# Kernel optimization log

Measured on AMD Instinct MI355X. Metric: run time of the kernel, lower is better.

The kernel has to match this reference:

```python
import math
import jax, jax.numpy as jnp
import numpy as np

I_DIM = 64
N_MODES = 16
FACTOR = 4
EPS = 1e-5


def group_norm(x, w, b):
    # x: [B, M, N, C] channels-last; torch GroupNorm(C//16, C) over (group_channels, M, N)
    B, M, N, C = x.shape
    g = C // 16
    xr = x.reshape(B, M, N, g, C // g)
    mean = xr.mean(axis=(1, 2, 4), keepdims=True)
    var = xr.var(axis=(1, 2, 4), keepdims=True)
    xr = (xr - mean) * jax.lax.rsqrt(var + EPS)
    return xr.reshape(B, M, N, C) * w + b


def feed_forward(x, res, l1w, l1b, l2w, l2b, g1w, g1b, g2w, g2b, g3w, g3b):
    h = x @ l1w + l1b                      # [B,M,N,C*factor]
    h = group_norm(h, g1w, g1b)            # fork_1
    h = jax.nn.relu(h)
    h = h @ l2w + l2b                      # [B,M,N,C]
    h = group_norm(h, g2w, g2b)            # fork_2
    h = res + h
    h = group_norm(h, g3w, g3b)            # fork_3
    return h


def setup_inputs() -> dict:
    key = jax.random.key(0)
    ks = jax.random.split(key, 20)
    B, M, N, I = 4, 128, 128, I_DIM
    H = I * FACTOR
    z = jax.random.normal(ks[0], (B, 2 * M * N * I, 1), dtype=jnp.float32)
    x = jax.random.normal(ks[1], (B, M * N * I, 1), dtype=jnp.float32)
    # fourier weights [in, out, nm, nm, 2], xavier-ish scale
    fw_scale = math.sqrt(2.0 / (I + I))
    fw1 = jax.random.normal(ks[2], (I, I, N_MODES, N_MODES, 2), dtype=jnp.float32) * fw_scale
    fw2 = jax.random.normal(ks[3], (I, I, N_MODES, N_MODES, 2), dtype=jnp.float32) * fw_scale
    def ff_params(k0):
        kk = jax.random.split(k0, 4)
        return dict(
            l1w=jax.random.normal(kk[0], (I, H), dtype=jnp.float32) * math.sqrt(2.0 / (I + H)),
            l1b=jnp.zeros((H,), jnp.float32),
            l2w=jax.random.normal(kk[1], (H, I), dtype=jnp.float32) * math.sqrt(2.0 / (I + H)),
            l2b=jnp.zeros((I,), jnp.float32),
            g1w=jnp.ones((H,), jnp.float32), g1b=jnp.zeros((H,), jnp.float32),
            g2w=jnp.ones((I,), jnp.float32), g2b=jnp.zeros((I,), jnp.float32),
            g3w=jnp.ones((I,), jnp.float32), g3b=jnp.zeros((I,), jnp.float32),
        )
    bp = ff_params(ks[4])
    fp = ff_params(ks[5])
    out = {"z": z, "x": x, "fw1": fw1, "fw2": fw2}
    for name, p in (("b", bp), ("f", fp)):
        for k, v in p.items():
            out[f"{name}_{k}"] = v
    return out


def reference(z, x, fw1, fw2,
              b_l1w, b_l1b, b_l2w, b_l2b, b_g1w, b_g1b, b_g2w, b_g2b, b_g3w, b_g3b,
              f_l1w, f_l1b, f_l2w, f_l2b, f_g1w, f_g1b, f_g2w, f_g2b, f_g3w, f_g3b):
    I = I_DIM
    nm = N_MODES
    B = x.shape[0]
    M = N = int(math.sqrt(x.shape[1] // I))
    x4 = x.reshape(B, M, N, I)
    z5 = z.reshape(B, 2, M, N, I)
    backcast, forecast = z5[:, 0], z5[:, 1]
    x4 = x4 - backcast
    xc = jnp.transpose(x4, (0, 3, 1, 2))          # [B, I, M, N]
    x_ft = jnp.fft.rfft2(xc, s=(M, N), norm='ortho')  # [B, I, M, N//2+1] complex64
    w1 = fw1[..., 0] + 1j * fw1[..., 1]
    w2 = fw2[..., 0] + 1j * fw2[..., 1]
    top = jnp.einsum('bixy,ioxy->boxy', x_ft[:, :, :nm, :nm], w1)
    bot = jnp.einsum('bixy,ioxy->boxy', x_ft[:, :, -nm:, :nm], w2)
    out_ft = jnp.zeros((B, I, N, M // 2 + 1), dtype=x_ft.dtype)
    out_ft = out_ft.at[:, :, :nm, :nm].set(top).at[:, :, -nm:, :nm].set(bot)
    xo = jnp.fft.irfft2(out_ft, s=(N, M), norm='ortho')  # [B, I, M, N]
    xo = jnp.transpose(xo, (0, 2, 3, 1))                  # [B, M, N, I]
    backcast = feed_forward(xo, backcast, b_l1w, b_l1b, b_l2w, b_l2b,
                            b_g1w, b_g1b, b_g2w, b_g2b, b_g3w, b_g3b)
    forecast = feed_forward(xo, forecast, f_l1w, f_l1b, f_l2w, f_l2b,
                            f_g1w, f_g1b, f_g2w, f_g2b, f_g3w, f_g3b)
    out = jnp.stack([backcast, forecast], axis=1)         # [B, 2, M, N, I]
    return out.reshape(B, 2 * M * N * I, 1)
```

## Files before the change

kernel.cpp:

```cpp
#include <hip/hip_runtime.h>
#include <hip/hip_bf16.h>

typedef __hip_bfloat16 bf16;
typedef __attribute__((ext_vector_type(8))) short short8;
typedef __attribute__((ext_vector_type(4))) float f32x4;

#define PI2 6.283185307179586f
#define EPSV 1e-5f

__device__ __forceinline__ short f2bs(float f){
  bf16 h = __float2bfloat16(f);
  short s; __builtin_memcpy(&s, &h, 2); return s;
}
__device__ __forceinline__ float s2f(short s){
  bf16 h; __builtin_memcpy(&h, &s, 2); return __bfloat162float(h);
}

__global__ __launch_bounds__(256) void k_prep(
    const float* __restrict__ fw1, const float* __restrict__ fw2,
    float2* __restrict__ FWT,
    const float* __restrict__ b_l1w, const float* __restrict__ b_l1b,
    const float* __restrict__ b_l2w, const float* __restrict__ b_l2b,
    const float* __restrict__ b_g1w, const float* __restrict__ b_g1b,
    const float* __restrict__ b_g2w, const float* __restrict__ b_g2b,
    const float* __restrict__ b_g3w, const float* __restrict__ b_g3b,
    const float* __restrict__ f_l1w, const float* __restrict__ f_l1b,
    const float* __restrict__ f_l2w, const float* __restrict__ f_l2b,
    const float* __restrict__ f_g1w, const float* __restrict__ f_g1b,
    const float* __restrict__ f_g2w, const float* __restrict__ f_g2b,
    const float* __restrict__ f_g3w, const float* __restrict__ f_g3b,
    short* __restrict__ W1g, short* __restrict__ W2g,
    float2* __restrict__ TWY, float2* __restrict__ TWX,
    float* __restrict__ PB, float* __restrict__ ST){
  __shared__ float Ls[16][512];
  int tid = threadIdx.x;
  if(blockIdx.x < 512){
    int arr = blockIdx.x >> 8, rem = blockIdx.x & 255;
    int i = rem >> 2, o0 = (rem & 3) * 16;
    const float* src = (arr ? fw2 : fw1) + ((size_t)(i*64 + o0))*512;
    for(int idx = tid; idx < 8192; idx += 256)
      Ls[idx >> 9][idx & 511] = src[idx];
    __syncthreads();
    int kxw = tid >> 4, ky = tid & 15;
    float2* dst = FWT + ((size_t)((arr*16 + kxw)*16 + ky))*4096 + i*64 + o0;
    for(int ol = 0; ol < 16; ol++)
      dst[ol] = make_float2(Ls[ol][tid*2], Ls[ol][tid*2 + 1]);
    return;
  }
  int i = (blockIdx.x - 512)*256 + tid;
  if(i < 32768){
    int br = i >> 14, r = i & 16383;
    int fid = r >> 9, lane = (r >> 3) & 63, e = r & 7;
    int hb = fid & 1, t = (fid >> 1) & 3, ch = fid >> 3;
    int l15 = lane & 15, quad = lane >> 4;
    int n = ch*64 + t*16 + l15;
    int k = hb*32 + quad*8 + e;
    const float* src = br ? f_l1w : b_l1w;
    W1g[i] = f2bs(src[k*256 + n]);
    return;
  }
  i -= 32768;
  if(i < 32768){
    int br = i >> 14, r = i & 16383;
    int fid = r >> 9, lane = (r >> 3) & 63, e = r & 7;
    int hb = fid & 1, t = (fid >> 1) & 3, ch = fid >> 3;
    int l15 = lane & 15, quad = lane >> 4;
    int n = t*16 + l15;
    int k = ch*64 + hb*32 + quad*8 + e;
    const float* src = br ? f_l2w : b_l2w;
    W2g[i] = f2bs(src[k*64 + n]);
    return;
  }
  i -= 32768;
  if(i < 2048){
    int ky = i >> 7, n = i & 127;
    float ang = PI2 * (float)((ky*n) & 127) / 128.0f;
    float s, c; sincosf(ang, &s, &c);
    TWY[i] = make_float2(c, s);
    return;
  }
  i -= 2048;
  if(i < 4096){
    int kp = i >> 7, m = i & 127;
    int kx = kp < 16 ? kp : 96 + kp;
    float ang = PI2 * (float)((kx*m) & 127) / 128.0f;
    float s, c; sincosf(ang, &s, &c);
    TWX[i] = make_float2(c, s);
    return;
  }
  i -= 4096;
  if(i < 384){ ST[i] = 0.f; return; }
  i -= 384;
  if(i < 2176){
    int br = i >= 1088; int o = i - br*1088;
    float* pb = PB + br*2048;
    float v;
    if(o < 256)       v = (br ? f_l1b : b_l1b)[o];
    else if(o < 512)  v = (br ? f_g1w : b_g1w)[o-256];
    else if(o < 768)  v = (br ? f_g1b : b_g1b)[o-512];
    else if(o < 832)  v = (br ? f_l2b : b_l2b)[o-768];
    else if(o < 896)  v = (br ? f_g2w : b_g2w)[o-832];
    else if(o < 960)  v = (br ? f_g2b : b_g2b)[o-896];
    else if(o < 1024) v = (br ? f_g3w : b_g3w)[o-960];
    else              v = (br ? f_g3b : b_g3b)[o-1024];
    pb[o] = v;
  }
}

__global__ __launch_bounds__(256) void k_ydft(const float* __restrict__ x,
                                              const float* __restrict__ z,
                                              const float2* __restrict__ TWY,
                                              float2* __restrict__ Y){
  __shared__ float Xs[128][64];
  __shared__ float2 twl[16][128];
  int b = blockIdx.x >> 7, m = blockIdx.x & 127;
  int tid = threadIdx.x;
  const float4* xp = (const float4*)(x + ((size_t)(b*128 + m)*128)*64);
  const float4* zp = (const float4*)(z + ((size_t)((b*2 + 0)*128 + m)*128)*64);
  float4* xs4 = (float4*)&Xs[0][0];
  for(int idx = tid; idx < 2048; idx += 256){
    float4 a = xp[idx], c = zp[idx];
    xs4[idx] = make_float4(a.x-c.x, a.y-c.y, a.z-c.z, a.w-c.w);
  }
  for(int idx = tid; idx < 2048; idx += 256)
    twl[idx >> 7][idx & 127] = TWY[idx];
  __syncthreads();
  int i = tid & 63, kq = tid >> 6;
  float re[4] = {0,0,0,0}, im[4] = {0,0,0,0};
  for(int n = 0; n < 128; n++){
    float v = Xs[n][i];
    #pragma unroll
    for(int j = 0; j < 4; j++){
      float2 t = twl[kq*4 + j][n];
      re[j] += v*t.x;
      im[j] -= v*t.y;
    }
  }
  #pragma unroll
  for(int j = 0; j < 4; j++)
    Y[((b*128 + m)*16 + kq*4 + j)*64 + i] = make_float2(re[j], im[j]);
}

__global__ __launch_bounds__(128) void k_xdft(const float2* __restrict__ Y,
                                              const float2* __restrict__ TWX,
                                              float2* __restrict__ X2){
  __shared__ float2 twl[16][128];
  int bi = blockIdx.x;
  int b = bi >> 6, ky = (bi >> 2) & 15, half = (bi >> 1) & 1, ih = bi & 1;
  int tid = threadIdx.x;
  for(int idx = tid; idx < 2048; idx += 128)
    twl[idx >> 7][idx & 127] = TWX[(half << 11) + idx];
  __syncthreads();
  int i = ih*32 + (tid & 31), grp = tid >> 5;
  float re[4], im[4];
  #pragma unroll
  for(int j = 0; j < 4; j++){ re[j] = 0.f; im[j] = 0.f; }
  #pragma unroll 4
  for(int m = 0; m < 128; m++){
    float2 y = Y[((b*128 + m)*16 + ky)*64 + i];
    #pragma unroll
    for(int j = 0; j < 4; j++){
      float2 t = twl[grp*4 + j][m];
      re[j] += y.x*t.x + y.y*t.y;
      im[j] += y.y*t.x - y.x*t.y;
    }
  }
  const float sc = 1.0f/128.0f;
  #pragma unroll
  for(int j = 0; j < 4; j++){
    int kp = half*16 + grp*4 + j;
    X2[((b*32 + kp)*16 + ky)*64 + i] = make_float2(re[j]*sc, im[j]*sc);
  }
}

__global__ __launch_bounds__(256) void k_mix(float2* __restrict__ X2,
                                             const float2* __restrict__ FWT){
  __shared__ float2 Xs[4][4][64];
  int tid = threadIdx.x;
  for(int idx = tid; idx < 1024; idx += 256){
    int pl = idx >> 8, b = (idx >> 6) & 3, i = idx & 63;
    int p = blockIdx.x*4 + pl; int kp = p >> 4, ky = p & 15;
    Xs[pl][b][i] = X2[((b*32 + kp)*16 + ky)*64 + i];
  }
  __syncthreads();
  int w = tid >> 6, o = tid & 63;
  int p = blockIdx.x*4 + w; int kp = p >> 4, ky = p & 15;
  int arr = kp < 16 ? 0 : 1, kxw = kp < 16 ? kp : kp - 16;
  const float2* wp = FWT + ((size_t)((arr*16 + kxw)*16 + ky))*4096;
  float rr[4] = {0,0,0,0}, ii[4] = {0,0,0,0};
  for(int i = 0; i < 64; i++){
    float2 wv = wp[i*64 + o];
    #pragma unroll
    for(int b = 0; b < 4; b++){
      float xr = Xs[w][b][i].x, xi = Xs[w][b][i].y;
      rr[b] += xr*wv.x - xi*wv.y;
      ii[b] += xr*wv.y + xi*wv.x;
    }
  }
  for(int b = 0; b < 4; b++)
    X2[((b*32 + kp)*16 + ky)*64 + o] = make_float2(rr[b], ii[b]);
}

__global__ __launch_bounds__(128) void k_inv1(const float2* __restrict__ OF,
                                              const float2* __restrict__ TWX,
                                              float2* __restrict__ T){
  __shared__ float2 F[32][32];
  __shared__ float2 twl[32][64];
  int bi = blockIdx.x;
  int b = bi >> 6, ky = (bi >> 2) & 15, mh = (bi >> 1) & 1, oh = bi & 1;
  int tid = threadIdx.x;
  for(int idx = tid; idx < 1024; idx += 128){
    int kp = idx >> 5, ol = idx & 31;
    F[kp][ol] = OF[((b*32 + kp)*16 + ky)*64 + oh*32 + ol];
  }
  for(int idx = tid; idx < 2048; idx += 128){
    int kp = idx >> 6, ml = idx & 63;
    twl[kp][ml] = TWX[kp*128 + mh*64 + ml];
  }
  __syncthreads();
  int ol = tid & 31, mg = tid >> 5;
  float re[16], im[16];
  #pragma unroll
  for(int u = 0; u < 16; u++){ re[u] = 0.f; im[u] = 0.f; }
  for(int kp = 0; kp < 32; kp++){
    float2 f = F[kp][ol];
    #pragma unroll
    for(int u = 0; u < 16; u++){
      float2 t = twl[kp][mg*16 + u];
      re[u] += f.x*t.x - f.y*t.y;
      im[u] += f.x*t.y + f.y*t.x;
    }
  }
  int o = oh*32 + ol;
  #pragma unroll
  for(int u = 0; u < 16; u++){
    int m = mh*64 + mg*16 + u;
    T[((b*128 + m)*16 + ky)*64 + o] = make_float2(re[u], im[u]);
  }
}

__global__ __launch_bounds__(256) void k_inv2(const float2* __restrict__ T,
                                              const float2* __restrict__ TWY,
                                              bf16* __restrict__ XO,
                                              float* __restrict__ CZ){
  __shared__ float2 twl[16][128];
  int b = blockIdx.x >> 7, m = blockIdx.x & 127;
  int tid = threadIdx.x;
  int flat = blockIdx.x*256 + tid;
  if(flat < 16640) CZ[flat] = 0.f;
  for(int idx = tid; idx < 2048; idx += 256)
    twl[idx >> 7][idx & 127] = TWY[idx];
  int o = tid & 63, ng = tid >> 6;
  const float2* tp = T + ((size_t)(b*128 + m)*16)*64 + o;
  float t0x = tp[0].x;
  float t2x[15], t2y[15];
  #pragma unroll
  for(int u = 0; u < 15; u++){
    float2 v = tp[(u + 1)*64];
    t2x[u] = 2.0f*v.x; t2y[u] = 2.0f*v.y;
  }
  __syncthreads();
  const float sc = 1.0f/128.0f;
  for(int n = ng*32; n < ng*32 + 32; n++){
    float v = t0x;
    #pragma unroll
    for(int u = 0; u < 15; u++){
      float2 t = twl[u + 1][n];
      v += t2x[u]*t.x - t2y[u]*t.y;
    }
    XO[((b*128 + m)*128 + n)*64 + o] = __float2bfloat16(v*sc);
  }
}

__global__ __launch_bounds__(256) void k_cov(const bf16* __restrict__ XO,
                                             float* __restrict__ Cg,
                                             float* __restrict__ SX){
  __shared__ short XT[64][264];
  __shared__ float sxl[64];
  int tid = threadIdx.x;
  int b = blockIdx.x >> 4, ck = blockIdx.x & 15;
  if(tid < 64) sxl[tid] = 0.f;
  float sxp[8];
  #pragma unroll
  for(int e = 0; e < 8; e++) sxp[e] = 0.f;
  int c0 = (tid & 7)*8;
  int lane = tid & 63, w = tid >> 6, l15 = lane & 15, quad = lane >> 4;
  f32x4 acc[4];
  #pragma unroll
  for(int tj = 0; tj < 4; tj++) acc[tj] = (f32x4){0.f,0.f,0.f,0.f};
  for(int st = 0; st < 4; st++){
    size_t pbase = (size_t)b*16384 + (size_t)ck*1024 + st*256;
    const short* xg = (const short*)XO + pbase*64;
    __syncthreads();
    for(int it = 0; it < 8; it++){
      int p = it*32 + (tid >> 3);
      short8 v = *(const short8*)(xg + (size_t)p*64 + c0);
      #pragma unroll
      for(int e = 0; e < 8; e++){
        XT[c0+e][p] = v[e];
        sxp[e] += s2f(v[e]);
      }
    }
    __syncthreads();
    for(int kk = 0; kk < 8; kk++){
      short8 a = *(const short8*)&XT[w*16 + l15][kk*32 + quad*8];
      #pragma unroll
      for(int tj = 0; tj < 4; tj++){
        short8 bfr = *(const short8*)&XT[tj*16 + l15][kk*32 + quad*8];
        acc[tj] = __builtin_amdgcn_mfma_f32_16x16x32_bf16(a, bfr, acc[tj], 0, 0, 0);
      }
    }
  }
  #pragma unroll
  for(int e = 0; e < 8; e++) atomicAdd(&sxl[c0+e], sxp[e]);
  __syncthreads();
  float* Cb = Cg + b*4096;
  #pragma unroll
  for(int tj = 0; tj < 4; tj++)
    #pragma unroll
    for(int r = 0; r < 4; r++)
      atomicAdd(&Cb[(w*16 + quad*4 + r)*64 + tj*16 + l15], acc[tj][r]);
  if(tid < 64) atomicAdd(&SX[b*64 + tid], sxl[tid]);
}

__global__ __launch_bounds__(256) void k_stat(const float* __restrict__ Cg,
                                              const float* __restrict__ SX,
                                              const short* __restrict__ W1g,
                                              const float* __restrict__ PB,
                                              float* __restrict__ ST){
  __shared__ float Cl[64][65];
  __shared__ float Wl[16][64];
  __shared__ float sxl[64];
  __shared__ float g2[2];
  int tid = threadIdx.x;
  int br = blockIdx.x >> 6, b = (blockIdx.x >> 4) & 3, g = blockIdx.x & 15;
  const float* Cb = Cg + b*4096;
  for(int u = tid; u < 4096; u += 256) Cl[u >> 6][u & 63] = Cb[u];
  const short* W1 = W1g + br*16384;
  for(int u = tid; u < 1024; u += 256){
    int nl = u >> 6, k = u & 63;
    int n = g*16 + nl;
    int fid = ((n >> 6)*4 + ((n >> 4) & 3))*2 + (k >> 5);
    int lane = ((k >> 3) & 3)*16 + (n & 15);
    Wl[nl][k] = s2f(W1[fid*512 + lane*8 + (k & 7)]);
  }
  if(tid < 64) sxl[tid] = SX[b*64 + tid];
  if(tid < 2) g2[tid] = 0.f;
  __syncthreads();
  int nl = tid >> 4, ic = tid & 15;
  float qa = 0.f, sa = 0.f;
  for(int io = 0; io < 4; io++){
    int i = ic*4 + io;
    float wi = Wl[nl][i];
    float dot = 0.f;
    #pragma unroll 8
    for(int j = 0; j < 64; j++) dot += Cl[i][j]*Wl[nl][j];
    qa += wi*dot;
    sa += wi*sxl[i];
  }
  for(int off = 8; off; off >>= 1){
    qa += __shfl_xor(qa, off);
    sa += __shfl_xor(sa, off);
  }
  if(ic == 0){
    float bn = PB[br*2048 + g*16 + nl];
    float hs = sa + 16384.f*bn;
    float hq = qa + 2.f*bn*sa + 16384.f*bn*bn;
    atomicAdd(&g2[0], hs); atomicAdd(&g2[1], hq);
  }
  __syncthreads();
  if(tid == 0){
    float* S1 = ST + br*192;
    S1[(b*16 + g)*2]     = g2[0];
    S1[(b*16 + g)*2 + 1] = g2[1];
  }
}

__global__ __launch_bounds__(256, 2) void k_ffmain(const bf16* __restrict__ XO,
                                                   const short* __restrict__ W1g,
                                                   const short* __restrict__ W2g,
                                                   const float* __restrict__ PB,
                                                   const float* __restrict__ ST,
                                                   const float* __restrict__ z,
                                                   float* __restrict__ CS,
                                                   float* __restrict__ out){
  __shared__ short Ws1[16384];
  __shared__ short Ws2[16384];
  __shared__ short Hn[64][72];
  __shared__ float mu1[16], rs1[16];
  __shared__ float cs[5][64];
  int tid = threadIdx.x;
  int br = blockIdx.x >> 8, rb = blockIdx.x & 255;
  int r0 = rb << 8, b = rb >> 6;
  const float* pb = PB + br*2048;
  {
    const uint4* g1 = (const uint4*)(W1g + br*16384);
    const uint4* g2w = (const uint4*)(W2g + br*16384);
    uint4* s1 = (uint4*)Ws1; uint4* s2 = (uint4*)Ws2;
    #pragma unroll
    for(int u = 0; u < 8; u++){
      s1[u*256 + tid] = g1[u*256 + tid];
      s2[u*256 + tid] = g2w[u*256 + tid];
    }
  }
  if(tid < 16){
    const float cnt = 262144.f;
    const float* S1 = ST + br*192;
    float s = S1[(b*16 + tid)*2], q = S1[(b*16 + tid)*2 + 1];
    float mean = s/cnt, var = q/cnt - mean*mean;
    mu1[tid] = mean; rs1[tid] = rsqrtf(fmaxf(var, 0.f) + EPSV);
  }
  {
    float* c1 = &cs[0][0];
    c1[tid] = 0.f;
    if(tid < 64) c1[256 + tid] = 0.f;
  }
  __syncthreads();
  int lane = tid & 63, w = tid >> 6, l15 = lane & 15, quad = lane >> 4;
  int myrow = w*16 + l15;
  float sh[4]  = {0,0,0,0}, sh2[4] = {0,0,0,0};
  float sz[4]  = {0,0,0,0}, sz2[4] = {0,0,0,0}, shz[4] = {0,0,0,0};
  for(int c = 0; c < 4; c++){
    const short* xop = (const short*)XO + ((size_t)(r0 + c*64 + myrow))*64;
    short8 a0 = *(const short8*)(xop + quad*8);
    short8 a1 = *(const short8*)(xop + 32 + quad*8);
    f32x4 acc2[4];
    #pragma unroll
    for(int t = 0; t < 4; t++) acc2[t] = (f32x4){0.f,0.f,0.f,0.f};
    for(int ch = 0; ch < 4; ch++){
      #pragma unroll
      for(int t = 0; t < 4; t++){
        int fid = (ch*4 + t)*2;
        short8 b0 = *(const short8*)(Ws1 + fid*512 + lane*8);
        short8 b1 = *(const short8*)(Ws1 + fid*512 + 512 + lane*8);
        f32x4 acc = {0.f,0.f,0.f,0.f};
        acc = __builtin_amdgcn_mfma_f32_16x16x32_bf16(a0, b0, acc, 0, 0, 0);
        acc = __builtin_amdgcn_mfma_f32_16x16x32_bf16(a1, b1, acc, 0, 0, 0);
        int n = ch*64 + t*16 + l15, gi = n >> 4;
        float w1v = pb[256 + n];
        float gwv = w1v * rs1[gi];
        float gbv = (pb[n] - mu1[gi])*rs1[gi]*w1v + pb[512 + n];
        #pragma unroll
        for(int r = 0; r < 4; r++){
          float hv = acc[r]*gwv + gbv;
          hv = hv > 0.f ? hv : 0.f;
          Hn[w*16 + quad*4 + r][t*16 + l15] = f2bs(hv);
        }
      }
      short8 ha0 = *(short8*)&Hn[myrow][quad*8];
      short8 ha1 = *(short8*)&Hn[myrow][32 + quad*8];
      #pragma unroll
      for(int t = 0; t < 4; t++){
        int fid = (ch*4 + t)*2;
        short8 b0 = *(const short8*)(Ws2 + fid*512 + lane*8);
        short8 b1 = *(const short8*)(Ws2 + fid*512 + 512 + lane*8);
        acc2[t] = __builtin_amdgcn_mfma_f32_16x16x32_bf16(ha0, b0, acc2[t], 0, 0, 0);
        acc2[t] = __builtin_amdgcn_mfma_f32_16x16x32_bf16(ha1, b1, acc2[t], 0, 0, 0);
      }
    }
    size_t obase_off = ((size_t)(b*2 + br)*16384 + (r0 & 16383) + c*64)*64;
    float* obase = out + obase_off;
    const float* zbase = z + obase_off;
    #pragma unroll
    for(int t = 0; t < 4; t++){
      int col = t*16 + l15;
      float bias2 = pb[768 + col];
      #pragma unroll
      for(int r = 0; r < 4; r++){
        size_t off = (size_t)(w*16 + quad*4 + r)*64 + col;
        float h2 = acc2[t][r] + bias2;
        float zv = zbase[off];
        obase[off] = h2;
        sh[t] += h2; sh2[t] += h2*h2;
        sz[t] += zv; sz2[t] += zv*zv; shz[t] += h2*zv;
      }
    }
  }
  #pragma unroll
  for(int t = 0; t < 4; t++){
    float v0 = sh[t], v1 = sh2[t], v2 = sz[t], v3 = sz2[t], v4 = shz[t];
    v0 += __shfl_xor(v0, 16); v0 += __shfl_xor(v0, 32);
    v1 += __shfl_xor(v1, 16); v1 += __shfl_xor(v1, 32);
    v2 += __shfl_xor(v2, 16); v2 += __shfl_xor(v2, 32);
    v3 += __shfl_xor(v3, 16); v3 += __shfl_xor(v3, 32);
    v4 += __shfl_xor(v4, 16); v4 += __shfl_xor(v4, 32);
    if(quad == 0){
      int ch = t*16 + l15;
      atomicAdd(&cs[0][ch], v0); atomicAdd(&cs[1][ch], v1);
      atomicAdd(&cs[2][ch], v2); atomicAdd(&cs[3][ch], v3);
      atomicAdd(&cs[4][ch], v4);
    }
  }
  __syncthreads();
  float* slab = CS + (size_t)blockIdx.x*320;
  const float* c1 = &cs[0][0];
  slab[tid] = c1[tid];
  if(tid < 64) slab[256 + tid] = c1[256 + tid];
}

__global__ __launch_bounds__(256) void k_statB(const float* __restrict__ CS,
                                               const float* __restrict__ PB,
                                               float* __restrict__ CF){
  __shared__ float chs[5][64];
  __shared__ float mu2s[4], rs2s[4], tg[4], tq[4], mu3s[4], rs3s[4];
  int br = blockIdx.x >> 2, b = blockIdx.x & 3;
  int tid = threadIdx.x;
  const float* base = CS + ((size_t)(br*256 + b*64))*320;
  float* c1 = &chs[0][0];
  for(int v = tid; v < 320; v += 256){
    float s = 0.f;
    for(int k = 0; k < 64; k++) s += base[(size_t)k*320 + v];
    c1[v] = s;
  }
  __syncthreads();
  if(tid < 4){
    float s = 0.f, q = 0.f;
    for(int o = tid*16; o < tid*16 + 16; o++){ s += chs[0][o]; q += chs[1][o]; }
    float mean = s/262144.f, var = q/262144.f - mean*mean;
    mu2s[tid] = mean; rs2s[tid] = rsqrtf(fmaxf(var, 0.f) + EPSV);
    tg[tid] = 0.f; tq[tid] = 0.f;
  }
  __syncthreads();
  const float* pb = PB + br*2048;
  if(tid < 64){
    int o = tid, g = o >> 4;
    float w2v = pb[832 + o], b2v = pb[896 + o];
    float gw = w2v*rs2s[g], gb = b2v - mu2s[g]*rs2s[g]*w2v;
    float Sh = chs[0][o], Sh2 = chs[1][o], Sz = chs[2][o], Sz2 = chs[3][o], Shz = chs[4][o];
    float st = gw*Sh + Sz + 16384.f*gb;
    float sq = gw*gw*Sh2 + Sz2 + 16384.f*gb*gb + 2.f*gw*Shz + 2.f*gw*gb*Sh + 2.f*gb*Sz;
    atomicAdd(&tg[g], st); atomicAdd(&tq[g], sq);
  }
  __syncthreads();
  if(tid < 4){
    float mean = tg[tid]/262144.f, var = tq[tid]/262144.f - mean*mean;
    mu3s[tid] = mean; rs3s[tid] = rsqrtf(fmaxf(var, 0.f) + EPSV);
  }
  __syncthreads();
  if(tid < 64){
    int o = tid, g = o >> 4;
    float w2v = pb[832 + o], b2v = pb[896 + o];
    float gw = w2v*rs2s[g], gb = b2v - mu2s[g]*rs2s[g]*w2v;
    float w3v = pb[960 + o], b3v = pb[1024 + o];
    float gw3 = w3v*rs3s[g], gb3 = b3v - mu3s[g]*rs3s[g]*w3v;
    float* cf = CF + (size_t)(br*4 + b)*192;
    cf[o]       = gw*gw3;
    cf[64 + o]  = gw3;
    cf[128 + o] = gb*gw3 + gb3;
  }
}

__global__ __launch_bounds__(256) void k_final(const float* __restrict__ z,
                                               const float* __restrict__ CF,
                                               float* __restrict__ out){
  int tid = blockIdx.x*256 + threadIdx.x;
  const float4* z4 = (const float4*)z;
  const float4* cf4 = (const float4*)CF;
  float4* o4 = (float4*)out;
  #pragma unroll
  for(int r = 0; r < 8; r++){
    int i4 = r*262144 + tid;
    int s = i4 >> 18;
    int b = s >> 1, br = s & 1;
    int cbase = (br*4 + b)*48 + (i4 & 15);
    float4 a = cf4[cbase], bb = cf4[cbase + 16], g = cf4[cbase + 32];
    float4 h = o4[i4], zv = z4[i4];
    o4[i4] = make_float4(h.x*a.x + zv.x*bb.x + g.x,
                         h.y*a.y + zv.y*bb.y + g.y,
                         h.z*a.z + zv.z*bb.z + g.z,
                         h.w*a.w + zv.w*bb.w + g.w);
  }
}

extern "C" void kernel_launch(void* const* d_in, const int* in_sizes, int n_in,
                              void* d_out, int out_size, void* d_ws, size_t ws_size,
                              hipStream_t stream){
  const float* z   = (const float*)d_in[0];
  const float* x   = (const float*)d_in[1];
  const float* fw1 = (const float*)d_in[2];
  const float* fw2 = (const float*)d_in[3];
  char* ws = (char*)d_ws;
  float2* Y   = (float2*)(ws + 0);
  float2* X2  = (float2*)(ws + 4194304);
  float2* T   = Y;
  bf16*   XO  = (bf16*)(ws + 5242880);
  float*  ST  = (float*)(ws + 13631488);
  short*  W1g = (short*)(ws + 13633536);
  short*  W2g = (short*)(ws + 13699072);
  float2* TWY = (float2*)(ws + 13764608);
  float2* TWX = (float2*)(ws + 13780992);
  float*  PB  = (float*)(ws + 13813760);
  float2* FWT = (float2*)(ws + 13830144);
  float*  Cg  = (float*)(ws + 13830144);
  float*  SX  = Cg + 16384;
  float*  CS  = (float*)(ws + 14878720);
  float*  CF  = (float*)(ws + 15927296);

  const float* p[20];
  for(int i = 0; i < 20; i++) p[i] = (const float*)d_in[4 + i];

  k_prep<<<802, 256, 0, stream>>>(fw1, fw2, FWT,
                                  p[0],p[1],p[2],p[3],p[4],p[5],p[6],p[7],p[8],p[9],
                                  p[10],p[11],p[12],p[13],p[14],p[15],p[16],p[17],p[18],p[19],
                                  W1g, W2g, TWY, TWX, PB, ST);
  k_ydft<<<512, 256, 0, stream>>>(x, z, TWY, Y);
  k_xdft<<<256, 128, 0, stream>>>(Y, TWX, X2);
  k_mix<<<128, 256, 0, stream>>>(X2, FWT);
  k_inv1<<<256, 128, 0, stream>>>(X2, TWX, T);
  k_inv2<<<512, 256, 0, stream>>>(T, TWY, XO, Cg);
  k_cov<<<64, 256, 0, stream>>>(XO, Cg, SX);
  k_stat<<<128, 256, 0, stream>>>(Cg, SX, W1g, PB, ST);
  k_ffmain<<<512, 256, 0, stream>>>(XO, W1g, W2g, PB, ST, z, CS, (float*)d_out);
  k_statB<<<8, 256, 0, stream>>>(CS, PB, CF);
  k_final<<<1024, 256, 0, stream>>>(z, CF, (float*)d_out);
}
```

Measured before the change: 299.5 us.

## Exploit DFT twiddle symmetries and split reductions across spectral stages

The forward y-DFT, x-DFT, inverse x-DFT and inverse y-DFT kernels now use twiddle periodicity (e.g. W^(k+N/2) and W^(N/4) structure) to fold inputs into sum and difference terms before the matmul-style DFT. This roughly halves or quarters the multiply-adds per output and shrinks the twiddle tables kept in shared memory. The x-DFT and mode-mixing kernels also split their reduction across two thread halves and combine the halves through shared memory, which raises thread counts and block counts. The cost is an extra sync and shared-memory combine, plus more complex indexing that must stay correct for the mode structure.

```diff
diff --git a/kernel.cpp b/kernel.cpp
--- a/kernel.cpp
+++ b/kernel.cpp
@@ -15,6 +15,8 @@
 __device__ __forceinline__ float s2f(short s){
   bf16 h; __builtin_memcpy(&h, &s, 2); return __bfloat162float(h);
 }
+__device__ __forceinline__ float4 f4add(float4 a, float4 b){ return make_float4(a.x+b.x, a.y+b.y, a.z+b.z, a.w+b.w); }
+__device__ __forceinline__ float4 f4sub(float4 a, float4 b){ return make_float4(a.x-b.x, a.y-b.y, a.z-b.z, a.w-b.w); }
 
 __global__ __launch_bounds__(256) void k_prep(
     const float* __restrict__ fw1, const float* __restrict__ fw2,
@@ -111,131 +113,170 @@
                                               const float* __restrict__ z,
                                               const float2* __restrict__ TWY,
                                               float2* __restrict__ Y){
-  __shared__ float Xs[128][64];
-  __shared__ float2 twl[16][128];
+  __shared__ float P[32][64], Q[32][64], R[32][64], S[32][64];
+  __shared__ float2 twl[16][32];
   int b = blockIdx.x >> 7, m = blockIdx.x & 127;
   int tid = threadIdx.x;
   const float4* xp = (const float4*)(x + ((size_t)(b*128 + m)*128)*64);
   const float4* zp = (const float4*)(z + ((size_t)((b*2 + 0)*128 + m)*128)*64);
-  float4* xs4 = (float4*)&Xs[0][0];
-  for(int idx = tid; idx < 2048; idx += 256){
-    float4 a = xp[idx], c = zp[idx];
-    xs4[idx] = make_float4(a.x-c.x, a.y-c.y, a.z-c.z, a.w-c.w);
-  }
-  for(int idx = tid; idx < 2048; idx += 256)
-    twl[idx >> 7][idx & 127] = TWY[idx];
+  int i4 = tid & 15, n0 = tid >> 4;
+  #pragma unroll
+  for(int it = 0; it < 2; it++){
+    int np = n0 + it*16;
+    float4 ea = f4sub(xp[np*16 + i4],      zp[np*16 + i4]);
+    float4 eb = f4sub(xp[(np+32)*16 + i4], zp[(np+32)*16 + i4]);
+    float4 ec = f4sub(xp[(np+64)*16 + i4], zp[(np+64)*16 + i4]);
+    float4 ed = f4sub(xp[(np+96)*16 + i4], zp[(np+96)*16 + i4]);
+    float4 sum_ac = f4add(ea, ec), sum_bd = f4add(eb, ed);
+    *(float4*)&P[np][i4*4] = f4add(sum_ac, sum_bd);
+    *(float4*)&Q[np][i4*4] = f4sub(sum_ac, sum_bd);
+    *(float4*)&R[np][i4*4] = f4sub(ea, ec);
+    *(float4*)&S[np][i4*4] = f4sub(eb, ed);
+  }
+  for(int idx = tid; idx < 512; idx += 256)
+    twl[idx >> 5][idx & 31] = TWY[(idx >> 5)*128 + (idx & 31)];
   __syncthreads();
   int i = tid & 63, kq = tid >> 6;
   float re[4] = {0,0,0,0}, im[4] = {0,0,0,0};
-  for(int n = 0; n < 128; n++){
-    float v = Xs[n][i];
-    #pragma unroll
-    for(int j = 0; j < 4; j++){
-      float2 t = twl[kq*4 + j][n];
-      re[j] += v*t.x;
-      im[j] -= v*t.y;
-    }
+  for(int np = 0; np < 32; np++){
+    float p = P[np][i], q = Q[np][i], r = R[np][i], s = S[np][i];
+    float2 t0 = twl[kq*4 + 0][np];
+    float2 t1 = twl[kq*4 + 1][np];
+    float2 t2 = twl[kq*4 + 2][np];
+    float2 t3 = twl[kq*4 + 3][np];
+    re[0] += p*t0.x;            im[0] -= p*t0.y;
+    re[1] += r*t1.x - s*t1.y;   im[1] -= s*t1.x + r*t1.y;
+    re[2] += q*t2.x;            im[2] -= q*t2.y;
+    re[3] += r*t3.x + s*t3.y;   im[3] += s*t3.x - r*t3.y;
   }
   #pragma unroll
   for(int j = 0; j < 4; j++)
     Y[((b*128 + m)*16 + kq*4 + j)*64 + i] = make_float2(re[j], im[j]);
 }
 
-__global__ __launch_bounds__(128) void k_xdft(const float2* __restrict__ Y,
+__global__ __launch_bounds__(256) void k_xdft(const float2* __restrict__ Y,
                                               const float2* __restrict__ TWX,
                                               float2* __restrict__ X2){
-  __shared__ float2 twl[16][128];
+  __shared__ float2 twl[16][64];
+  __shared__ float sc[128][8];
   int bi = blockIdx.x;
   int b = bi >> 6, ky = (bi >> 2) & 15, half = (bi >> 1) & 1, ih = bi & 1;
   int tid = threadIdx.x;
-  for(int idx = tid; idx < 2048; idx += 128)
-    twl[idx >> 7][idx & 127] = TWX[(half << 11) + idx];
-  __syncthreads();
-  int i = ih*32 + (tid & 31), grp = tid >> 5;
-  float re[4], im[4];
-  #pragma unroll
-  for(int j = 0; j < 4; j++){ re[j] = 0.f; im[j] = 0.f; }
-  #pragma unroll 4
-  for(int m = 0; m < 128; m++){
-    float2 y = Y[((b*128 + m)*16 + ky)*64 + i];
+  for(int idx = tid; idx < 1024; idx += 256)
+    twl[idx >> 6][idx & 63] = TWX[(half*16 + (idx >> 6))*128 + (idx & 63)];
+  __syncthreads();
+  int i = ih*32 + (tid & 31), grp = (tid >> 5) & 3, mh2 = tid >> 7;
+  const float2* yb = Y + (size_t)b*131072 + ky*64 + i;
+  float re[4] = {0,0,0,0}, im[4] = {0,0,0,0};
+  for(int mi = 0; mi < 32; mi++){
+    int mp = mh2*32 + mi;
+    float2 y1 = yb[(size_t)mp*1024];
+    float2 y2 = yb[(size_t)(mp + 64)*1024];
+    float2 ye = make_float2(y1.x + y2.x, y1.y + y2.y);
+    float2 yo = make_float2(y1.x - y2.x, y1.y - y2.y);
+    float2 t0 = twl[grp*4 + 0][mp];
+    float2 t1 = twl[grp*4 + 1][mp];
+    float2 t2 = twl[grp*4 + 2][mp];
+    float2 t3 = twl[grp*4 + 3][mp];
+    re[0] += ye.x*t0.x + ye.y*t0.y;  im[0] += ye.y*t0.x - ye.x*t0.y;
+    re[1] += yo.x*t1.x + yo.y*t1.y;  im[1] += yo.y*t1.x - yo.x*t1.y;
+    re[2] += ye.x*t2.x + ye.y*t2.y;  im[2] += ye.y*t2.x - ye.x*t2.y;
+    re[3] += yo.x*t3.x + yo.y*t3.y;  im[3] += yo.y*t3.x - yo.x*t3.y;
+  }
+  if(mh2){
+    int sl = tid & 127;
+    #pragma unroll
+    for(int j = 0; j < 4; j++){ sc[sl][j] = re[j]; sc[sl][4 + j] = im[j]; }
+  }
+  __syncthreads();
+  if(!mh2){
+    const float scn = 1.0f/128.0f;
     #pragma unroll
     for(int j = 0; j < 4; j++){
-      float2 t = twl[grp*4 + j][m];
-      re[j] += y.x*t.x + y.y*t.y;
-      im[j] += y.y*t.x - y.x*t.y;
-    }
-  }
-  const float sc = 1.0f/128.0f;
-  #pragma unroll
-  for(int j = 0; j < 4; j++){
-    int kp = half*16 + grp*4 + j;
-    X2[((b*32 + kp)*16 + ky)*64 + i] = make_float2(re[j]*sc, im[j]*sc);
+      float rr = (re[j] + sc[tid][j])*scn;
+      float ii = (im[j] + sc[tid][4 + j])*scn;
+      int kp = half*16 + grp*4 + j;
+      X2[((b*32 + kp)*16 + ky)*64 + i] = make_float2(rr, ii);
+    }
   }
 }
 
 __global__ __launch_bounds__(256) void k_mix(float2* __restrict__ X2,
                                              const float2* __restrict__ FWT){
-  __shared__ float2 Xs[4][4][64];
-  int tid = threadIdx.x;
-  for(int idx = tid; idx < 1024; idx += 256){
+  __shared__ float2 Xs[2][4][64];
+  __shared__ float sc[2][64][8];
+  int tid = threadIdx.x;
+  for(int idx = tid; idx < 512; idx += 256){
     int pl = idx >> 8, b = (idx >> 6) & 3, i = idx & 63;
-    int p = blockIdx.x*4 + pl; int kp = p >> 4, ky = p & 15;
+    int p = blockIdx.x*2 + pl; int kp = p >> 4, ky = p & 15;
     Xs[pl][b][i] = X2[((b*32 + kp)*16 + ky)*64 + i];
   }
   __syncthreads();
-  int w = tid >> 6, o = tid & 63;
-  int p = blockIdx.x*4 + w; int kp = p >> 4, ky = p & 15;
+  int o = tid & 63, w = tid >> 6, pl = w >> 1, ih = w & 1;
+  int p = blockIdx.x*2 + pl; int kp = p >> 4, ky = p & 15;
   int arr = kp < 16 ? 0 : 1, kxw = kp < 16 ? kp : kp - 16;
   const float2* wp = FWT + ((size_t)((arr*16 + kxw)*16 + ky))*4096;
   float rr[4] = {0,0,0,0}, ii[4] = {0,0,0,0};
-  for(int i = 0; i < 64; i++){
+  for(int i = ih*32; i < ih*32 + 32; i++){
     float2 wv = wp[i*64 + o];
     #pragma unroll
     for(int b = 0; b < 4; b++){
-      float xr = Xs[w][b][i].x, xi = Xs[w][b][i].y;
+      float xr = Xs[pl][b][i].x, xi = Xs[pl][b][i].y;
       rr[b] += xr*wv.x - xi*wv.y;
       ii[b] += xr*wv.y + xi*wv.x;
     }
   }
-  for(int b = 0; b < 4; b++)
-    X2[((b*32 + kp)*16 + ky)*64 + o] = make_float2(rr[b], ii[b]);
-}
-
-__global__ __launch_bounds__(128) void k_inv1(const float2* __restrict__ OF,
+  if(ih){
+    #pragma unroll
+    for(int b = 0; b < 4; b++){ sc[pl][o][b*2] = rr[b]; sc[pl][o][b*2 + 1] = ii[b]; }
+  }
+  __syncthreads();
+  if(!ih){
+    #pragma unroll
+    for(int b = 0; b < 4; b++){
+      float r2 = rr[b] + sc[pl][o][b*2], i2 = ii[b] + sc[pl][o][b*2 + 1];
+      X2[((b*32 + kp)*16 + ky)*64 + o] = make_float2(r2, i2);
+    }
+  }
+}
+
+__global__ __launch_bounds__(256) void k_inv1(const float2* __restrict__ OF,
                                               const float2* __restrict__ TWX,
                                               float2* __restrict__ T){
-  __shared__ float2 F[32][32];
+  __shared__ float2 Fl[32][16];
   __shared__ float2 twl[32][64];
   int bi = blockIdx.x;
-  int b = bi >> 6, ky = (bi >> 2) & 15, mh = (bi >> 1) & 1, oh = bi & 1;
-  int tid = threadIdx.x;
-  for(int idx = tid; idx < 1024; idx += 128){
-    int kp = idx >> 5, ol = idx & 31;
-    F[kp][ol] = OF[((b*32 + kp)*16 + ky)*64 + oh*32 + ol];
-  }
-  for(int idx = tid; idx < 2048; idx += 128){
+  int b = bi >> 6, ky = (bi >> 2) & 15, oq = bi & 3;
+  int tid = threadIdx.x;
+  for(int idx = tid; idx < 512; idx += 256){
+    int kp = idx >> 4, ol = idx & 15;
+    Fl[kp][ol] = OF[((b*32 + kp)*16 + ky)*64 + oq*16 + ol];
+  }
+  for(int idx = tid; idx < 2048; idx += 256){
     int kp = idx >> 6, ml = idx & 63;
-    twl[kp][ml] = TWX[kp*128 + mh*64 + ml];
-  }
-  __syncthreads();
-  int ol = tid & 31, mg = tid >> 5;
-  float re[16], im[16];
-  #pragma unroll
-  for(int u = 0; u < 16; u++){ re[u] = 0.f; im[u] = 0.f; }
-  for(int kp = 0; kp < 32; kp++){
-    float2 f = F[kp][ol];
-    #pragma unroll
-    for(int u = 0; u < 16; u++){
-      float2 t = twl[kp][mg*16 + u];
-      re[u] += f.x*t.x - f.y*t.y;
-      im[u] += f.x*t.y + f.y*t.x;
-    }
-  }
-  int o = oh*32 + ol;
-  #pragma unroll
-  for(int u = 0; u < 16; u++){
-    int m = mh*64 + mg*16 + u;
-    T[((b*128 + m)*16 + ky)*64 + o] = make_float2(re[u], im[u]);
+    twl[kp][ml] = TWX[kp*128 + ml];
+  }
+  __syncthreads();
+  int ol = tid & 15, mg = tid >> 4;
+  float reE[4] = {0,0,0,0}, imE[4] = {0,0,0,0};
+  float reO[4] = {0,0,0,0}, imO[4] = {0,0,0,0};
+  for(int kp = 0; kp < 32; kp += 2){
+    float2 fe = Fl[kp][ol], fo = Fl[kp + 1][ol];
+    #pragma unroll
+    for(int u = 0; u < 4; u++){
+      float2 te = twl[kp][mg*4 + u], to = twl[kp + 1][mg*4 + u];
+      reE[u] += fe.x*te.x - fe.y*te.y;
+      imE[u] += fe.x*te.y + fe.y*te.x;
+      reO[u] += fo.x*to.x - fo.y*to.y;
+      imO[u] += fo.x*to.y + fo.y*to.x;
+    }
+  }
+  int o = oq*16 + ol;
+  #pragma unroll
+  for(int u = 0; u < 4; u++){
+    int ml = mg*4 + u;
+    T[((b*128 + ml)*16 + ky)*64 + o]      = make_float2(reE[u] + reO[u], imE[u] + imO[u]);
+    T[((b*128 + ml + 64)*16 + ky)*64 + o] = make_float2(reE[u] - reO[u], imE[u] - imO[u]);
   }
 }
 
@@ -243,32 +284,42 @@
                                               const float2* __restrict__ TWY,
                                               bf16* __restrict__ XO,
                                               float* __restrict__ CZ){
-  __shared__ float2 twl[16][128];
-  int b = blockIdx.x >> 7, m = blockIdx.x & 127;
+  __shared__ float2 twl[16][64];
+  int b = blockIdx.x >> 6, mp = blockIdx.x & 63;
+  int m0 = mp*2, m1 = m0 + 1;
   int tid = threadIdx.x;
   int flat = blockIdx.x*256 + tid;
   if(flat < 16640) CZ[flat] = 0.f;
-  for(int idx = tid; idx < 2048; idx += 256)
-    twl[idx >> 7][idx & 127] = TWY[idx];
+  for(int idx = tid; idx < 1024; idx += 256)
+    twl[idx >> 6][idx & 63] = TWY[(idx >> 6)*128 + (idx & 63)];
   int o = tid & 63, ng = tid >> 6;
-  const float2* tp = T + ((size_t)(b*128 + m)*16)*64 + o;
-  float t0x = tp[0].x;
-  float t2x[15], t2y[15];
+  const float2* tp0 = T + ((size_t)(b*128 + m0)*16)*64 + o;
+  const float2* tp1 = T + ((size_t)(b*128 + m1)*16)*64 + o;
+  float t0a = tp0[0].x, t0b = tp1[0].x;
+  float ax[15], ay[15], bx2[15], by2[15];
   #pragma unroll
   for(int u = 0; u < 15; u++){
-    float2 v = tp[(u + 1)*64];
-    t2x[u] = 2.0f*v.x; t2y[u] = 2.0f*v.y;
-  }
-  __syncthreads();
-  const float sc = 1.0f/128.0f;
-  for(int n = ng*32; n < ng*32 + 32; n++){
-    float v = t0x;
+    float2 v0 = tp0[(u + 1)*64]; ax[u]  = 2.f*v0.x; ay[u]  = 2.f*v0.y;
+    float2 v1 = tp1[(u + 1)*64]; bx2[u] = 2.f*v1.x; by2[u] = 2.f*v1.y;
+  }
+  __syncthreads();
+  const float scn = 1.0f/128.0f;
+  bf16* xo0 = XO + ((size_t)(b*128 + m0)*128)*64 + o;
+  bf16* xo1 = XO + ((size_t)(b*128 + m1)*128)*64 + o;
+  for(int np = ng*16; np < ng*16 + 16; np++){
+    float A0 = t0a, B0 = 0.f, A1 = t0b, B1 = 0.f;
     #pragma unroll
     for(int u = 0; u < 15; u++){
-      float2 t = twl[u + 1][n];
-      v += t2x[u]*t.x - t2y[u]*t.y;
-    }
-    XO[((b*128 + m)*128 + n)*64 + o] = __float2bfloat16(v*sc);
+      float2 t = twl[u + 1][np];
+      float pr0 = ax[u]*t.x  - ay[u]*t.y;
+      float pr1 = bx2[u]*t.x - by2[u]*t.y;
+      if(u & 1){ A0 += pr0; A1 += pr1; }
+      else     { B0 += pr0; B1 += pr1; }
+    }
+    xo0[(size_t)np*64]        = __float2bfloat16((A0 + B0)*scn);
+    xo0[(size_t)(np + 64)*64] = __float2bfloat16((A0 - B0)*scn);
+    xo1[(size_t)np*64]        = __float2bfloat16((A1 + B1)*scn);
+    xo1[(size_t)(np + 64)*64] = __float2bfloat16((A1 - B1)*scn);
   }
 }
 
@@ -604,10 +655,10 @@
                                   p[10],p[11],p[12],p[13],p[14],p[15],p[16],p[17],p[18],p[19],
                                   W1g, W2g, TWY, TWX, PB, ST);
   k_ydft<<<512, 256, 0, stream>>>(x, z, TWY, Y);
-  k_xdft<<<256, 128, 0, stream>>>(Y, TWX, X2);
-  k_mix<<<128, 256, 0, stream>>>(X2, FWT);
-  k_inv1<<<256, 128, 0, stream>>>(X2, TWX, T);
-  k_inv2<<<512, 256, 0, stream>>>(T, TWY, XO, Cg);
+  k_xdft<<<256, 256, 0, stream>>>(Y, TWX, X2);
+  k_mix<<<256, 256, 0, stream>>>(X2, FWT);
+  k_inv1<<<256, 256, 0, stream>>>(X2, TWX, T);
+  k_inv2<<<256, 256, 0, stream>>>(T, TWY, XO, Cg);
   k_cov<<<64, 256, 0, stream>>>(XO, Cg, SX);
   k_stat<<<128, 256, 0, stream>>>(Cg, SX, W1g, PB, ST);
   k_ffmain<<<512, 256, 0, stream>>>(XO, W1g, W2g, PB, ST, z, CS, (float*)d_out);
```

New measurement: 261.7 us. -12.6%, faster.
